# Kernel tuning notes

Measured on AMD Instinct MI355X. Metric: run time of the kernel, lower is better.

The kernel has to match this reference:

```python
import jax, jax.numpy as jnp
import numpy as np

B, T, D, H = 8, 1024, 512, 8
QD, PD, POSD, VD, K = 32, 4, 48, 64, 31
FF = 4 * D
FF1, FF2, FF3, NLA = FF * 3 // 4, FF, FF * 5 // 4, D * 3 // 4


def _swoosh_l(x):
    return jax.nn.softplus(x - 4.0) - 0.08 * x - 0.035


def _swoosh_r(x):
    return jax.nn.softplus(x - 1.0) - 0.08 * x - 0.313261687


def setup_inputs() -> dict:
    key = jax.random.key(0)
    ks = iter(jax.random.split(key, 64))

    def w(shape, fan_in):
        return jax.random.normal(next(ks), shape, jnp.float32) * (fan_in ** -0.5)

    inp = {
        'x': jax.random.normal(next(ks), (B, T, D), jnp.float32),
        'pos_emb': jax.random.normal(next(ks), (2 * T - 1, POSD), jnp.float32),
        'mask': jnp.ones((B, T), bool),
        'attw_q_w': w((D, H * QD), D), 'attw_k_w': w((D, H * QD), D),
        'attw_pq_w': w((D, H * PD), D), 'attw_pos_w': w((POSD, H * PD), POSD),
        'ff1_in_w': w((D, FF1), D), 'ff1_in_b': jnp.zeros(FF1),
        'ff1_out_w': w((FF1, D), FF1), 'ff1_out_b': jnp.zeros(D),
        'nla_w': w((D, NLA * 3), D), 'nla_b': jnp.zeros(NLA * 3),
        'nla_out_w': w((NLA, D), NLA), 'nla_out_b': jnp.zeros(D),
        'sa1_v_w': w((D, H * VD), D), 'sa1_v_b': jnp.zeros(H * VD),
        'sa1_o_w': w((H * VD, D), H * VD), 'sa1_o_b': jnp.zeros(D),
        'conv1_in_w': w((D, 2 * D), D), 'conv1_in_b': jnp.zeros(2 * D),
        'conv1_dw_w': w((D, 1, K), K), 'conv1_dw_b': jnp.zeros(D),
        'conv1_out_w': w((D, D), D), 'conv1_out_b': jnp.zeros(D),
        'ff2_in_w': w((D, FF2), D), 'ff2_in_b': jnp.zeros(FF2),
        'ff2_out_w': w((FF2, D), FF2), 'ff2_out_b': jnp.zeros(D),
        'mid_scale': jax.random.uniform(next(ks), (D,), jnp.float32),
        'sa2_v_w': w((D, H * VD), D), 'sa2_v_b': jnp.zeros(H * VD),
        'sa2_o_w': w((H * VD, D), H * VD), 'sa2_o_b': jnp.zeros(D),
        'conv2_in_w': w((D, 2 * D), D), 'conv2_in_b': jnp.zeros(2 * D),
        'conv2_dw_w': w((D, 1, K), K), 'conv2_dw_b': jnp.zeros(D),
        'conv2_out_w': w((D, D), D), 'conv2_out_b': jnp.zeros(D),
        'ff3_in_w': w((D, FF3), D), 'ff3_in_b': jnp.zeros(FF3),
        'ff3_out_w': w((FF3, D), FF3), 'ff3_out_b': jnp.zeros(D),
        'norm_bias': jnp.zeros(D), 'norm_log_scale': jnp.zeros(()),
        'out_scale': jax.random.uniform(next(ks), (D,), jnp.float32),
    }
    return inp


def _forward(x, pos_emb, attw_q_w, attw_k_w, attw_pq_w, attw_pos_w,
             ff1_in_w, ff1_in_b, ff1_out_w, ff1_out_b,
             nla_w, nla_b, nla_out_w, nla_out_b,
             sa1_v_w, sa1_v_b, sa1_o_w, sa1_o_b,
             conv1_in_w, conv1_in_b, conv1_dw_w, conv1_dw_b, conv1_out_w, conv1_out_b,
             ff2_in_w, ff2_in_b, ff2_out_w, ff2_out_b,
             mid_scale,
             sa2_v_w, sa2_v_b, sa2_o_w, sa2_o_b,
             conv2_in_w, conv2_in_b, conv2_dw_w, conv2_dw_b, conv2_out_w, conv2_out_b,
             ff3_in_w, ff3_in_b, ff3_out_w, ff3_out_b,
             norm_bias, norm_log_scale, out_scale, mask):
    res = x
    # --- relative-pos multi-head attention weights ---
    q = (x @ attw_q_w).reshape(B, T, H, QD).transpose(0, 2, 1, 3)
    k = (x @ attw_k_w).reshape(B, T, H, QD).transpose(0, 2, 1, 3)
    p = (x @ attw_pq_w).reshape(B, T, H, PD).transpose(0, 2, 1, 3)
    content = jnp.einsum('bhtd,bhsd->bhts', q, k) * (QD ** -0.5)
    rel = (pos_emb @ attw_pos_w).reshape(2 * T - 1, H, PD).transpose(1, 0, 2)
    idx = jnp.arange(T)[:, None] - jnp.arange(T)[None, :] + (T - 1)
    relg = rel[:, idx]  # [H, T, T, PD]
    scores = content + jnp.einsum('bhtd,htsd->bhts', p, relg)
    scores = jnp.where(mask[:, None, None, :], scores, -10000.0)
    attn = jax.nn.softmax(scores, axis=-1)
    attn = jnp.where(mask[:, None, :, None], attn, 0.0)

    def mk(y):
        return jnp.where(mask[..., None], y, 0.0)

    def ff(y, wi, bi, wo, bo):
        return _swoosh_l(y @ wi + bi) @ wo + bo

    def sa(y, vw, vb, ow, ob):
        v = (y @ vw + vb).reshape(B, T, H, VD).transpose(0, 2, 1, 3)
        o = jnp.einsum('bhts,bhsd->bhtd', attn, v).transpose(0, 2, 1, 3).reshape(B, T, H * VD)
        return o @ ow + ob

    def conv(y, iw, ib, dw, db, ow, ob):
        u = y @ iw + ib
        a, g = jnp.split(u, 2, axis=-1)
        a = (a * jax.nn.sigmoid(g)).transpose(0, 2, 1)  # [B, D, T]
        a = jnp.where(mask[:, None, :], a, 0.0)
        c = jax.lax.conv_general_dilated(a, dw, (1,), [(K // 2, K // 2)],
                                         dimension_numbers=('NCH', 'OIH', 'NCH'),
                                         feature_group_count=D) + db[None, :, None]
        c = _swoosh_r(c.transpose(0, 2, 1))
        return mk(c @ ow + ob)

    def bypass(r, u, s):
        s = jnp.clip(s, 0.2, 1.0)  # eval/steady regime
        return r + (u - r) * s

    x = mk(x + ff(x, ff1_in_w, ff1_in_b, ff1_out_w, ff1_out_b))
    # non-linear attention (uses head 0)
    a, b, c = jnp.split(x @ nla_w + nla_b, 3, axis=-1)
    att0 = jnp.einsum('bts,bsd->btd', attn[:, 0], jnp.tanh(b) * c)
    x = mk(x + ((a * att0) @ nla_out_w + nla_out_b))
    x = mk(x + sa(x, sa1_v_w, sa1_v_b, sa1_o_w, sa1_o_b))
    x = mk(x + conv(x, conv1_in_w, conv1_in_b, conv1_dw_w, conv1_dw_b, conv1_out_w, conv1_out_b))
    x = mk(x + ff(x, ff2_in_w, ff2_in_b, ff2_out_w, ff2_out_b))
    x = mk(bypass(res, x, mid_scale))
    x = mk(x + sa(x, sa2_v_w, sa2_v_b, sa2_o_w, sa2_o_b))
    x = mk(x + conv(x, conv2_in_w, conv2_in_b, conv2_dw_w, conv2_dw_b, conv2_out_w, conv2_out_b))
    x = mk(x + ff(x, ff3_in_w, ff3_in_b, ff3_out_w, ff3_out_b))
    # BiasNorm
    rms = jnp.sqrt(jnp.mean((x - norm_bias) ** 2, axis=-1, keepdims=True) + 1e-8)
    x = x / rms * jnp.exp(norm_log_scale)
    x = mk(bypass(res, x, out_scale))
    return x


def reference(x, pos_emb, mask, attw_q_w, attw_k_w, attw_pq_w, attw_pos_w,
              ff1_in_w, ff1_in_b, ff1_out_w, ff1_out_b,
              nla_w, nla_b, nla_out_w, nla_out_b,
              sa1_v_w, sa1_v_b, sa1_o_w, sa1_o_b,
              conv1_in_w, conv1_in_b, conv1_dw_w, conv1_dw_b, conv1_out_w, conv1_out_b,
              ff2_in_w, ff2_in_b, ff2_out_w, ff2_out_b,
              mid_scale,
              sa2_v_w, sa2_v_b, sa2_o_w, sa2_o_b,
              conv2_in_w, conv2_in_b, conv2_dw_w, conv2_dw_b, conv2_out_w, conv2_out_b,
              ff3_in_w, ff3_in_b, ff3_out_w, ff3_out_b,
              norm_bias, norm_log_scale, out_scale):
    return _forward(x, pos_emb, attw_q_w, attw_k_w, attw_pq_w, attw_pos_w,
                    ff1_in_w, ff1_in_b, ff1_out_w, ff1_out_b,
                    nla_w, nla_b, nla_out_w, nla_out_b,
                    sa1_v_w, sa1_v_b, sa1_o_w, sa1_o_b,
                    conv1_in_w, conv1_in_b, conv1_dw_w, conv1_dw_b, conv1_out_w, conv1_out_b,
                    ff2_in_w, ff2_in_b, ff2_out_w, ff2_out_b,
                    mid_scale,
                    sa2_v_w, sa2_v_b, sa2_o_w, sa2_o_b,
                    conv2_in_w, conv2_in_b, conv2_dw_w, conv2_dw_b, conv2_out_w, conv2_out_b,
                    ff3_in_w, ff3_in_b, ff3_out_w, ff3_out_b,
                    norm_bias, norm_log_scale, out_scale, mask)
```

## Files before the change

kernel.cpp:

```cpp
#include <hip/hip_runtime.h>
#include <hip/hip_bf16.h>
#include <math.h>

using bf16 = __hip_bfloat16;
using f16 = _Float16;
typedef short s16x8 __attribute__((ext_vector_type(8)));
typedef f16   f16x2 __attribute__((ext_vector_type(2)));
typedef float f32x4 __attribute__((ext_vector_type(4)));
typedef unsigned int u32;
#define DEV __device__ __forceinline__
#define AS1 __attribute__((address_space(1)))
#define AS3 __attribute__((address_space(3)))

constexpr int Bc = 8, Tc = 1024, Dc = 512, Hc = 8;
constexpr int QDc = 32, PDc = 4, POSDc = 48, VDc = 64;
constexpr int Nrow = Bc * Tc;
constexpr int KWc = 31;

DEV float frcp(float x) { return __builtin_amdgcn_rcpf(x); }
DEV float softplus_f(float y) { return fmaxf(y, 0.f) + __logf(1.f + __expf(-fabsf(y))); }
DEV float swoosh_l_f(float x) { return softplus_f(x - 4.f) - 0.08f * x - 0.035f; }
DEV float swoosh_r_f(float x) { return softplus_f(x - 1.f) - 0.08f * x - 0.313261687f; }
DEV float sigmoid_f(float x)  { return frcp(1.f + __expf(-x)); }
DEV float tanh_f(float x) {
  float e = __expf(2.f * fminf(fmaxf(x, -15.f), 15.f));
  return (e - 1.f) * frcp(e + 1.f);
}
DEV float clip_s(float s)     { return fminf(fmaxf(s, 0.2f), 1.0f); }
DEV float to_f(bf16 x)  { return __bfloat162float(x); }
DEV float b2f(short s) { union { u32 u; float f; } z; z.u = (u32)(unsigned short)s << 16; return z.f; }
DEV short f2bb(float v) { bf16 h = __float2bfloat16(v); return *(short*)&h; }
DEV unsigned short f2h(float v) { f16 h = (f16)v; union { f16 x; unsigned short s; } z; z.x = h; return z.s; }
DEV float h2f(unsigned short s) { union { unsigned short s; f16 x; } z; z.s = s; return (float)z.x; }
DEV u32 packbf(float a, float b) {
  return ((u32)(unsigned short)f2bb(b) << 16) | (u32)(unsigned short)f2bb(a);
}
DEV float dot2(u32 a, u32 b, float c) {
#if __has_builtin(__builtin_amdgcn_fdot2)
  union { u32 u; f16x2 v; } x, y; x.u = a; y.u = b;
  return __builtin_amdgcn_fdot2(x.v, y.v, c, false);
#else
  return c + h2f(a & 0xffff) * h2f(b & 0xffff) + h2f(a >> 16) * h2f(b >> 16);
#endif
}

DEV float wave_max(float v) {
#pragma unroll
  for (int o = 32; o > 0; o >>= 1) v = fmaxf(v, __shfl_xor(v, o));
  return v;
}
DEV float wave_sum(float v) {
#pragma unroll
  for (int o = 32; o > 0; o >>= 1) v += __shfl_xor(v, o);
  return v;
}

DEV void gload16(const void* g, void* l) {
  __builtin_amdgcn_global_load_lds((const AS1 u32*)g, (AS3 u32*)l, 16, 0, 0);
}

#define SWZ(a) ((a) ^ ((((a) >> 7) & 7) << 4))

template <int ACT, int WM, int WN, int FM, int FN>
__global__ __launch_bounds__(256) void gemm_mfma(
    const bf16* __restrict__ A, const bf16* __restrict__ B,
    const float* __restrict__ bias, const float* __restrict__ resid,
    float* __restrict__ Cf, bf16* __restrict__ Cb, bf16* __restrict__ Cb2,
    int M, int N, int K, int lda, int ldb, int ldc,
    long sAz, long sBo, long sBi, long sCo, long sCi, int nh) {
  constexpr int BM = WM * FM * 16, BN = WN * FN * 16;
  constexpr int NP = (ACT == 2) ? 2 : (ACT == 3) ? 3 : 1;
  constexpr int PANOFF = (ACT == 2) ? 512 : 384;
  constexpr int ASZ = BM * 128, BUF = (BM + NP * BN) * 128;
  constexpr int LPS = BM / 32 + NP * (BN / 32);

  int z = blockIdx.z;
  int zo = z / nh, zi = z - zo * nh;
  A += (long)z * sAz;
  B += (long)zo * sBo + (long)zi * sBi;
  long coff = (long)zo * sCo + (long)zi * sCi;

  __shared__ char lds[2 * BUF];

  int tid = threadIdx.x;
  int lane = tid & 63, w = tid >> 6;
  int wm = w / WN, wn = w % WN;

  int gx = gridDim.x;
  int nwg = gx * gridDim.y;
  int flat = blockIdx.y * gx + blockIdx.x;
  if ((nwg & 7) == 0) flat = (flat & 7) * (nwg >> 3) + (flat >> 3);
  int m0 = (flat / gx) * BM, n0 = (flat % gx) * BN;

  int lrow = lane >> 3, lch = lane & 7;
  const bf16* ga = A + (long)(m0 + w * (BM / 4) + lrow) * lda + ((lch ^ lrow) << 3);
  const bf16* gb = B + (long)(n0 + w * (BN / 4) + lrow) * ldb + ((lch ^ lrow) << 3);

  f32x4 acc[NP][FM][FN];
#pragma unroll
  for (int p = 0; p < NP; ++p)
#pragma unroll
    for (int i = 0; i < FM; ++i)
#pragma unroll
      for (int j = 0; j < FN; ++j) acc[p][i][j] = 0.f;

  int nt = K >> 6;
  {
    char* la = lds + w * (BM / 4) * 128;
#pragma unroll
    for (int i = 0; i < BM / 32; ++i) gload16(ga + (long)(i * 8) * lda, la + i * 1024);
#pragma unroll
    for (int p = 0; p < NP; ++p) {
      const bf16* gp = gb + (long)(p * PANOFF) * ldb;
      char* lb = lds + ASZ + p * BN * 128 + w * (BN / 4) * 128;
#pragma unroll
      for (int i = 0; i < BN / 32; ++i) gload16(gp + (long)(i * 8) * ldb, lb + i * 1024);
    }
  }

  for (int t = 0; t < nt; ++t) {
// ... 21 lines not shown
    for (int ks = 0; ks < 2; ++ks) {
      int cg = ks * 4 + (lane >> 4);
      s16x8 af[FM];
#pragma unroll
      for (int f = 0; f < FM; ++f) {
        int row = wm * FM * 16 + f * 16 + (lane & 15);
        af[f] = *(const s16x8*)(cA + row * 128 + ((cg ^ (row & 7)) << 4));
      }
#pragma unroll
      for (int p = 0; p < NP; ++p) {
        char* cB = cA + ASZ + p * BN * 128;
        s16x8 bfr[FN];
#pragma unroll
        for (int f = 0; f < FN; ++f) {
          int row = wn * FN * 16 + f * 16 + (lane & 15);
          bfr[f] = *(const s16x8*)(cB + row * 128 + ((cg ^ (row & 7)) << 4));
        }
#pragma unroll
        for (int fm = 0; fm < FM; ++fm)
#pragma unroll
          for (int fn = 0; fn < FN; ++fn)
            acc[p][fm][fn] = __builtin_amdgcn_mfma_f32_16x16x32_bf16(
                af[fm], bfr[fn], acc[p][fm][fn], 0, 0, 0);
      }
    }
    __builtin_amdgcn_sched_barrier(0);
    __builtin_amdgcn_s_barrier();
  }

  int rbase = m0 + wm * FM * 16 + (lane >> 4) * 4;
  int cbase = n0 + wn * FN * 16 + (lane & 15);
#pragma unroll
  for (int fn = 0; fn < FN; ++fn) {
    int col = cbase + fn * 16;
    if (col >= N) continue;
    float bv = bias ? bias[col] : 0.f;
#pragma unroll
    for (int fm = 0; fm < FM; ++fm) {
#pragma unroll
      for (int r = 0; r < 4; ++r) {
        int row = rbase + fm * 16 + r;
        if (row >= M) continue;
        long ci = coff + (long)row * ldc + col;
        if constexpr (ACT == 2) {
          float va = acc[0][fm][fn][r] + bv;
          float vg = acc[1][fm][fn][r] + bias[col + 512];
          Cb[ci] = __float2bfloat16(va * sigmoid_f(vg));
        } else if constexpr (ACT == 3) {
          float va = acc[0][fm][fn][r] + bv;
          float vb = acc[1][fm][fn][r] + bias[col + 384];
          float vc = acc[2][fm][fn][r] + bias[col + 768];
          Cb2[ci] = __float2bfloat16(va);
          Cb[ci] = __float2bfloat16(tanh_f(vb) * vc);
        } else {
          float v = acc[0][fm][fn][r] + bv;
          if (ACT == 1) v = swoosh_l_f(v);
          if (resid) v += resid[ci];
          if (Cf) Cf[ci] = v;
          if (Cb) Cb[ci] = __float2bfloat16(v);
        }
      }
    }
  }
}

__global__ __launch_bounds__(256) void gemm_mfma_nt(
    const bf16* __restrict__ A, const bf16* __restrict__ B,
    bf16* __restrict__ Cb, int M, int N, int K, int lda, int ldb, int ldc,
    long sAz, long sBo, long sCo) {
  int z = blockIdx.z;
  A += (long)z * sAz;
  B += (long)z * sBo;
  long coff = (long)z * sCo;

  __shared__ char lds[32768];
  char* Al = lds;
  char* Bl = lds + 16384;

  int tid = threadIdx.x;
  int lane = tid & 63, w = tid >> 6;
  int wm = w >> 1, wn = w & 1;
  int m0 = blockIdx.y * 128, n0 = blockIdx.x * 128;

  f32x4 acc[4][4];
#pragma unroll
  for (int i = 0; i < 4; ++i)
#pragma unroll
    for (int j = 0; j < 4; ++j) acc[i][j] = 0.f;

  for (int k0 = 0; k0 < K; k0 += 64) {
#pragma unroll
    for (int i = 0; i < 4; ++i) {
      int flat = tid + i * 256;
      int row = flat >> 3, ch = flat & 7;
      uint4 v = {0, 0, 0, 0};
      if (m0 + row < M)
        v = *(const uint4*)(A + (long)(m0 + row) * lda + k0 + ch * 8);
      *(uint4*)(Al + SWZ(row * 128 + ch * 16)) = v;
    }
#pragma unroll
    for (int i = 0; i < 4; ++i) {
      int flat = tid + i * 256;
      int kk = flat >> 4, nc = flat & 15;
      if (n0 + nc * 8 < N) {
        uint4 v = *(const uint4*)(B + (long)(k0 + kk) * ldb + n0 + nc * 8);
        const unsigned short* pv = (const unsigned short*)&v;
#pragma unroll
        for (int j = 0; j < 8; ++j)
          *(unsigned short*)(Bl + SWZ((nc * 8 + j) * 128 + kk * 2)) = pv[j];
      }
    }
    __syncthreads();
#pragma unroll
    for (int ks = 0; ks < 2; ++ks) {
      s16x8 af[4], bfr[4];
#pragma unroll
      for (int f = 0; f < 4; ++f)
        af[f] = *(const s16x8*)(Al + SWZ((wm * 64 + f * 16 + (lane & 15)) * 128 +
                                         ks * 64 + (lane >> 4) * 16));
#pragma unroll
      for (int f = 0; f < 4; ++f)
        bfr[f] = *(const s16x8*)(Bl + SWZ((wn * 64 + f * 16 + (lane & 15)) * 128 +
                                          ks * 64 + (lane >> 4) * 16));
#pragma unroll
      for (int fm = 0; fm < 4; ++fm)
#pragma unroll
        for (int fn = 0; fn < 4; ++fn)
          acc[fm][fn] = __builtin_amdgcn_mfma_f32_16x16x32_bf16(
              af[fm], bfr[fn], acc[fm][fn], 0, 0, 0);
    }
    __syncthreads();
  }

  int rbase = m0 + wm * 64 + (lane >> 4) * 4;
  int cbase = n0 + wn * 64 + (lane & 15);
#pragma unroll
  for (int fn = 0; fn < 4; ++fn) {
    int col = cbase + fn * 16;
    if (col >= N) continue;
#pragma unroll
    for (int fm = 0; fm < 4; ++fm) {
#pragma unroll
      for (int r = 0; r < 4; ++r) {
        int row = rbase + fm * 16 + r;
        if (row >= M) continue;
        Cb[coff + (long)row * ldc + col] = __float2bfloat16(acc[fm][fn][r]);
      }
    }
  }
}

__global__ __launch_bounds__(256) void gemm_tile_f32(
    const float* __restrict__ A, const float* __restrict__ Bm,
    float* __restrict__ Cf, f16* __restrict__ Ch,
    int M, int N, int K, int lda, int ldb, int ldc) {
  __shared__ float As[16][72];
  __shared__ float Bs[16][72];
  int tid = threadIdx.x;
  int tx = tid & 15, ty = tid >> 4;
  int m0 = blockIdx.y * 64, n0 = blockIdx.x * 64;
  int arow = tid >> 2, ak4 = (tid & 3) * 4;
  int bk = tid >> 4, bn4 = (tid & 15) * 4;
  float acc[4][4] = {};
  for (int k0 = 0; k0 < K; k0 += 16) {
    int gm = m0 + arow;
#pragma unroll
    for (int j = 0; j < 4; ++j) {
      int gk = k0 + ak4 + j;
      As[ak4 + j][arow] = (gm < M && gk < K) ? A[(long)gm * lda + gk] : 0.f;
    }
    int gk = k0 + bk;
#pragma unroll
    for (int j = 0; j < 4; ++j) {
      int gn = n0 + bn4 + j;
      Bs[bk][bn4 + j] = (gk < K && gn < N) ? Bm[(long)gk * ldb + gn] : 0.f;
    }
    __syncthreads();
#pragma unroll
    for (int kk = 0; kk < 16; ++kk) {
      float a4[4], b4[4];
#pragma unroll
      for (int i = 0; i < 4; ++i) a4[i] = As[kk][ty * 4 + i];
#pragma unroll
      for (int i = 0; i < 4; ++i) b4[i] = Bs[kk][tx * 4 + i];
#pragma unroll
      for (int i = 0; i < 4; ++i)
#pragma unroll
        for (int j = 0; j < 4; ++j) acc[i][j] += a4[i] * b4[j];
    }
    __syncthreads();
  }
#pragma unroll
  for (int i = 0; i < 4; ++i) {
    int gm = m0 + ty * 4 + i;
    if (gm >= M) continue;
#pragma unroll
    for (int j = 0; j < 4; ++j) {
      int gn = n0 + tx * 4 + j;
      if (gn < N) {
// ... 41 lines not shown
  __shared__ short t[64][72];
  int bx = blockIdx.x * 64;
  int by = blockIdx.y * 64;
  int tid = threadIdx.x;
  int r = tid >> 3, c8 = tid & 7;
#pragma unroll
  for (int p = 0; p < 2; ++p) {
    s16x8 v = *(const s16x8*)((const short*)src + (long)(bx + p * 32 + r) * C + by + c8 * 8);
#pragma unroll
    for (int j = 0; j < 8; ++j) t[p * 32 + r][c8 * 8 + j] = v[j];
  }
  __syncthreads();
  int j = tid >> 2, q = tid & 3;
  s16x8 o0, o1;
#pragma unroll
  for (int e = 0; e < 8; ++e) o0[e] = t[q * 16 + e][j];
#pragma unroll
  for (int e = 0; e < 8; ++e) o1[e] = t[q * 16 + 8 + e][j];
  short* dp = (short*)dst + (long)(by + j) * R + bx + q * 16;
  *(s16x8*)dp = o0;
  *(s16x8*)(dp + 8) = o1;
}

__global__ void dw_transpose_kernel(const float* __restrict__ dw1, float* __restrict__ o1,
                                    const float* __restrict__ dw2, float* __restrict__ o2) {
  int i = blockIdx.x * 256 + threadIdx.x;
  if (i >= 2 * 512 * KWc) return;
  const float* s = (i < 512 * KWc) ? dw1 : dw2;
  float* o = (i < 512 * KWc) ? o1 : o2;
  int j = (i < 512 * KWc) ? i : i - 512 * KWc;
  int d = j / KWc, kk = j - d * KWc;
  o[kk * 512 + d] = s[j];
}

__global__ void f2b_kernel(const float* __restrict__ in, bf16* __restrict__ out, int nOct) {
  int i = blockIdx.x * 256 + threadIdx.x;
  if (i >= nOct) return;
  float4 a = *(const float4*)(in + (long)i * 8);
  float4 b = *(const float4*)(in + (long)i * 8 + 4);
  s16x8 o;
  o[0] = f2bb(a.x); o[1] = f2bb(a.y); o[2] = f2bb(a.z); o[3] = f2bb(a.w);
  o[4] = f2bb(b.x); o[5] = f2bb(b.y); o[6] = f2bb(b.z); o[7] = f2bb(b.w);
  *(s16x8*)((short*)out + (long)i * 8) = o;
}

__global__ __launch_bounds__(256) void scores_softmax_fused(
    const bf16* __restrict__ qk, const f16* __restrict__ ph,
    const float* __restrict__ rel, bf16* __restrict__ attn) {
  int bh = blockIdx.y;
  int h = bh & (Hc - 1), b = bh >> 3;
  int t0 = blockIdx.x * 16;
  int tid = threadIdx.x, lane = tid & 63, w = tid >> 6;

  __shared__ unsigned short scS[16 * 1024];
  __shared__ u32 rel01[1040], rel23[1040];
  __shared__ u32 pS[16][2];
  __shared__ float mS[16][4];

  for (int i = tid; i < 1039; i += 256) {
    float4 rv = *(const float4*)(rel + (long)(t0 + i) * 32 + h * 4);
    rel01[i] = ((u32)f2h(rv.y) << 16) | f2h(rv.x);
    rel23[i] = ((u32)f2h(rv.w) << 16) | f2h(rv.z);
  }
  if (tid < 16) {
    const u32* pp = (const u32*)(ph + ((long)(b * Tc + t0 + tid)) * 32 + h * 4);
    pS[tid][0] = pp[0]; pS[tid][1] = pp[1];
  }
  __syncthreads();

  s16x8 af = *(const s16x8*)(qk + ((long)(b * Tc + t0 + (lane & 15))) * 512 +
                             h * QDc + (lane >> 4) * 8);
  int g = lane >> 4;
  u32 p01[4], p23[4];
#pragma unroll
  for (int r = 0; r < 4; ++r) { p01[r] = pS[g * 4 + r][0]; p23[r] = pS[g * 4 + r][1]; }
  float mx[4] = {-3e38f, -3e38f, -3e38f, -3e38f};
  f32x4 zero = {0.f, 0.f, 0.f, 0.f};
  int cols0 = w * 256;
#pragma unroll 4
  for (int tile = 0; tile < 16; ++tile) {
    int s0 = cols0 + tile * 16;
    s16x8 bfr = *(const s16x8*)(qk + ((long)(b * Tc + s0 + (lane & 15))) * 512 +
                                256 + h * QDc + (lane >> 4) * 8);
    f32x4 acc = __builtin_amdgcn_mfma_f32_16x16x32_bf16(af, bfr, zero, 0, 0, 0);
    int scol = s0 + (lane & 15);
    int idx0 = g * 4 - scol + 1023;
#pragma unroll
    for (int r = 0; r < 4; ++r) {
      int idx = idx0 + r;
      float pos = dot2(p23[r], rel23[idx], dot2(p01[r], rel01[idx], 0.f));
      float v = acc[r] + pos;
      mx[r] = fmaxf(mx[r], v);
      *(unsigned short*)((char*)scS + (g * 4 + r) * 2048 + ((scol * 2) ^ (g << 5))) = f2h(v);
    }
  }
#pragma unroll
  for (int o = 1; o < 16; o <<= 1)
#pragma unroll
    for (int r = 0; r < 4; ++r) mx[r] = fmaxf(mx[r], __shfl_xor(mx[r], o));
  if ((lane & 15) == 0) {
#pragma unroll
    for (int r = 0; r < 4; ++r) mS[g * 4 + r][w] = mx[r];
  }
  __syncthreads();

#pragma unroll
  for (int rr = 0; rr < 4; ++rr) {
    int row = w * 4 + rr;
    float mf = fmaxf(fmaxf(mS[row][0], mS[row][1]), fmaxf(mS[row][2], mS[row][3]));
    int mask = ((row >> 2) & 3) << 5;
    char* rowbase = (char*)scS + row * 2048;
    float e[16];
    float lsum = 0.f;
#pragma unroll
    for (int k = 0; k < 8; ++k) {
      u32 cw = *(u32*)(rowbase + (((lane + k * 64) * 4) ^ mask));
      float e0 = __expf(h2f(cw & 0xffff) - mf);
      float e1 = __expf(h2f(cw >> 16) - mf);
      e[k * 2] = e0; e[k * 2 + 1] = e1;
      lsum += e0 + e1;
    }
    lsum = wave_sum(lsum);
    float inv = frcp(lsum);
    u32* grow = (u32*)(attn + ((long)bh * Tc + t0 + row) * Tc);
#pragma unroll
    for (int k = 0; k < 8; ++k)
      grow[lane + k * 64] = packbf(e[k * 2] * inv, e[k * 2 + 1] * inv);
  }
}

__global__ void amul_kernel(const bf16* __restrict__ a, bf16* __restrict__ io, int nOct) {
  int i = blockIdx.x * 256 + threadIdx.x;
  if (i >= nOct) return;
  s16x8 av = *(const s16x8*)((const short*)a + (long)i * 8);
  short* p = (short*)io + (long)i * 8;
  s16x8 v = *(const s16x8*)p;
#pragma unroll
  for (int j = 0; j < 8; ++j) v[j] = f2bb(b2f(v[j]) * b2f(av[j]));
  *(s16x8*)p = v;
}

__global__ void bypass_kernel(const float* __restrict__ r, const float* __restrict__ u,
                              const float* __restrict__ s, float* __restrict__ out,
                              bf16* __restrict__ outb, int nOct) {
  int i = blockIdx.x * 256 + threadIdx.x;
  if (i >= nOct) return;
  int d0 = (i & 63) * 8;
  long base = (long)i * 8;
  float4 r0 = *(const float4*)(r + base), r1 = *(const float4*)(r + base + 4);
  float4 u0 = *(const float4*)(u + base), u1 = *(const float4*)(u + base + 4);
  float4 s0 = *(const float4*)(s + d0),  s1 = *(const float4*)(s + d0 + 4);
  float4 o0, o1;
  o0.x = r0.x + (u0.x - r0.x) * clip_s(s0.x);
  o0.y = r0.y + (u0.y - r0.y) * clip_s(s0.y);
  o0.z = r0.z + (u0.z - r0.z) * clip_s(s0.z);
  o0.w = r0.w + (u0.w - r0.w) * clip_s(s0.w);
  o1.x = r1.x + (u1.x - r1.x) * clip_s(s1.x);
  o1.y = r1.y + (u1.y - r1.y) * clip_s(s1.y);
  o1.z = r1.z + (u1.z - r1.z) * clip_s(s1.z);
  o1.w = r1.w + (u1.w - r1.w) * clip_s(s1.w);
  *(float4*)(out + base) = o0;
  *(float4*)(out + base + 4) = o1;
  s16x8 ob;
  ob[0] = f2bb(o0.x); ob[1] = f2bb(o0.y); ob[2] = f2bb(o0.z); ob[3] = f2bb(o0.w);
  ob[4] = f2bb(o1.x); ob[5] = f2bb(o1.y); ob[6] = f2bb(o1.z); ob[7] = f2bb(o1.w);
  *(s16x8*)((short*)outb + base) = ob;
}

__global__ __launch_bounds__(256) void dwconv_kernel(
    const bf16* __restrict__ a, const float* __restrict__ dwT,
    const float* __restrict__ db, bf16* __restrict__ c) {
  int i = blockIdx.x * 256 + threadIdx.x;
  int oct = i & 63, bt = i >> 6;
  int t = bt & (Tc - 1), b0 = bt - t;
  float acc0 = db[oct * 8 + 0], acc1 = db[oct * 8 + 1], acc2 = db[oct * 8 + 2],
        acc3 = db[oct * 8 + 3], acc4 = db[oct * 8 + 4], acc5 = db[oct * 8 + 5],
        acc6 = db[oct * 8 + 6], acc7 = db[oct * 8 + 7];
#pragma unroll
  for (int kk = 0; kk < KWc; ++kk) {
    int tt = t + kk - (KWc / 2);
    if ((unsigned)tt < (unsigned)Tc) {
      s16x8 av = *(const s16x8*)((const short*)a + ((long)(b0 + tt) << 9) + oct * 8);
      const float* wp = dwT + kk * 512 + oct * 8;
      float4 w0 = *(const float4*)wp, w1 = *(const float4*)(wp + 4);
      acc0 += b2f(av[0]) * w0.x; acc1 += b2f(av[1]) * w0.y;
      acc2 += b2f(av[2]) * w0.z; acc3 += b2f(av[3]) * w0.w;
      acc4 += b2f(av[4]) * w1.x; acc5 += b2f(av[5]) * w1.y;
      acc6 += b2f(av[6]) * w1.z; acc7 += b2f(av[7]) * w1.w;
    }
  }
  s16x8 o;
  o[0] = f2bb(swoosh_r_f(acc0)); o[1] = f2bb(swoosh_r_f(acc1));
  o[2] = f2bb(swoosh_r_f(acc2)); o[3] = f2bb(swoosh_r_f(acc3));
  o[4] = f2bb(swoosh_r_f(acc4)); o[5] = f2bb(swoosh_r_f(acc5));
  o[6] = f2bb(swoosh_r_f(acc6)); o[7] = f2bb(swoosh_r_f(acc7));
  *(s16x8*)((short*)c + (long)bt * 512 + oct * 8) = o;
}

__global__ __launch_bounds__(256) void rmsnorm_bypass_kernel(
    const float* __restrict__ x, const float* __restrict__ x0,
    const float* __restrict__ nb, const float* __restrict__ nls,
    const float* __restrict__ os, float* __restrict__ out) {
  int row = blockIdx.x;
  int tid = threadIdx.x;
  const float* xr = x + (long)row * 512;
  const float* rr = x0 + (long)row * 512;
  float* orow = out + (long)row * 512;
  float v0 = xr[tid], v1 = xr[tid + 256];
  float d0 = v0 - nb[tid], d1 = v1 - nb[tid + 256];
  float ss = d0 * d0 + d1 * d1;
  __shared__ float red[4];
  int lane = tid & 63, wid = tid >> 6;
  ss = wave_sum(ss);
  if (lane == 0) red[wid] = ss;
  __syncthreads();
  ss = red[0] + red[1] + red[2] + red[3];
  float rms = sqrtf(ss * (1.f / 512.f) + 1e-8f);
  float scl = expf(nls[0]) / rms;
  float r0 = rr[tid], s0 = clip_s(os[tid]);
  orow[tid] = r0 + (v0 * scl - r0) * s0;
  float r1 = rr[tid + 256], s1 = clip_s(os[tid + 256]);
  orow[tid + 256] = r1 + (v1 * scl - r1) * s1;
}

static inline int cdiv(int a, int b) { return (a + b - 1) / b; }

template <int ACT, int WM = 2, int WN = 2, int FM = 2, int FN = 2>
static void mfma_launch(hipStream_t st, const bf16* A, const bf16* B, const float* bias,
                        const float* resid, float* Cf, bf16* Cb, bf16* Cb2,
                        int M, int N, int K, int lda, int ldb, int ldc,
                        int Z = 1, int nh = 1, long sAz = 0, long sBo = 0, long sBi = 0,
                        long sCo = 0, long sCi = 0) {
  dim3 grid(cdiv(N, WN * FN * 16), cdiv(M, WM * FM * 16), Z);
  gemm_mfma<ACT, WM, WN, FM, FN><<<grid, dim3(256), 0, st>>>(
      A, B, bias, resid, Cf, Cb, Cb2, M, N, K, lda, ldb, ldc,
      sAz, sBo, sBi, sCo, sCi, nh);
}
#define MFMA_AV 4, 1, 2, 4

extern "C" void kernel_launch(void* const* d_in, const int* in_sizes, int n_in,
                              void* d_out, int out_size, void* d_ws, size_t ws_size,
                              hipStream_t stream) {
  const float* x0        = (const float*)d_in[0];
  const float* pos_emb   = (const float*)d_in[1];
  const float* Wq        = (const float*)d_in[3];
  const float* Wk        = (const float*)d_in[4];
  const float* Wpq       = (const float*)d_in[5];
  const float* Wpos      = (const float*)d_in[6];
  const float* ff1_in_w  = (const float*)d_in[7];
  const float* ff1_in_b  = (const float*)d_in[8];
  const float* ff1_out_w = (const float*)d_in[9];
  const float* ff1_out_b = (const float*)d_in[10];
  const float* nla_w     = (const float*)d_in[11];
  const float* nla_b     = (const float*)d_in[12];
  const float* nla_out_w = (const float*)d_in[13];
  const float* nla_out_b = (const float*)d_in[14];
  const float* sa1_v_w   = (const float*)d_in[15];
  const float* sa1_v_b   = (const float*)d_in[16];
  const float* sa1_o_w   = (const float*)d_in[17];
  const float* sa1_o_b   = (const float*)d_in[18];
  const float* cv1_in_w  = (const float*)d_in[19];
  const float* cv1_in_b  = (const float*)d_in[20];
  const float* cv1_dw_w  = (const float*)d_in[21];
  const float* cv1_dw_b  = (const float*)d_in[22];
  const float* cv1_out_w = (const float*)d_in[23];
  const float* cv1_out_b = (const float*)d_in[24];
  const float* ff2_in_w  = (const float*)d_in[25];
  const float* ff2_in_b  = (const float*)d_in[26];
  const float* ff2_out_w = (const float*)d_in[27];
  const float* ff2_out_b = (const float*)d_in[28];
  const float* mid_scale = (const float*)d_in[29];
  const float* sa2_v_w   = (const float*)d_in[30];
  const float* sa2_v_b   = (const float*)d_in[31];
  const float* sa2_o_w   = (const float*)d_in[32];
  const float* sa2_o_b   = (const float*)d_in[33];
  const float* cv2_in_w  = (const float*)d_in[34];
  const float* cv2_in_b  = (const float*)d_in[35];
  const float* cv2_dw_w  = (const float*)d_in[36];
  const float* cv2_dw_b  = (const float*)d_in[37];
  const float* cv2_out_w = (const float*)d_in[38];
  const float* cv2_out_b = (const float*)d_in[39];
  const float* ff3_in_w  = (const float*)d_in[40];
  const float* ff3_in_b  = (const float*)d_in[41];
  const float* ff3_out_w = (const float*)d_in[42];
  const float* ff3_out_b = (const float*)d_in[43];
  const float* norm_bias = (const float*)d_in[44];
  const float* nls       = (const float*)d_in[45];
  const float* out_scale = (const float*)d_in[46];
  float* out = (float*)d_out;

  char* wsb = (char*)d_ws;
  size_t off = 0;
  bf16* attn  = (bf16*)(wsb + off); off += (size_t)Bc * Hc * Tc * Tc * 2;
  float* xA   = (float*)(wsb + off); off += (size_t)Nrow * Dc * 4;
  float* xB   = (float*)(wsb + off); off += (size_t)Nrow * Dc * 4;
  bf16*  xb   = (bf16*)(wsb + off);  off += (size_t)Nrow * Dc * 2;
  bf16*  x0b  = (bf16*)(wsb + off);  off += (size_t)Nrow * Dc * 2;
  bf16*  big1b = (bf16*)(wsb + off); off += (size_t)Nrow * 2560 * 2;
  bf16*  big2b = (bf16*)(wsb + off); off += (size_t)Nrow * Dc * 2;
  bf16*  wT    = (bf16*)(wsb + off); off += (size_t)9961472 * 2;
  float* dwT1  = (float*)(wsb + off); off += (size_t)KWc * 512 * 4;
  float* dwT2  = (float*)(wsb + off); off += (size_t)KWc * 512 * 4;
  bf16* big3b = big1b + (size_t)Nrow * 2048;
  bf16* vT    = big2b;
  bf16* qk    = big1b;
  bf16* abuf  = big1b;
  f16*  ph    = (f16*)(big1b + (size_t)Nrow * 512);
  float* relb = (float*)(ph + (size_t)Nrow * 32);

  bf16* p_w = wT;
  auto alloc_w = [&](int n, int k) { bf16* r = p_w; p_w += (size_t)n * k; return r; };
  bf16* ff1_in_wT  = alloc_w(1536, 512);
  bf16* ff1_out_wT = alloc_w(512, 1536);
  bf16* nla_wT     = alloc_w(1152, 512);
  bf16* nla_out_wT = alloc_w(512, 384);
  bf16* sa1_v_wT   = alloc_w(512, 512);
  bf16* sa1_o_wT   = alloc_w(512, 512);
  bf16* cv1_in_wT  = alloc_w(1024, 512);
  bf16* cv1_out_wT = alloc_w(512, 512);
  bf16* ff2_in_wT  = alloc_w(2048, 512);
  bf16* ff2_out_wT = alloc_w(512, 2048);
  bf16* sa2_v_wT   = alloc_w(512, 512);
  bf16* sa2_o_wT   = alloc_w(512, 512);
  bf16* cv2_in_wT  = alloc_w(1024, 512);
  bf16* cv2_out_wT = alloc_w(512, 512);
  bf16* ff3_in_wT  = alloc_w(2560, 512);
  bf16* ff3_out_wT = alloc_w(512, 2560);
  bf16* WqkT       = alloc_w(512, 512);

  const int nOctD  = Nrow * 64;
  const int nOct384 = Nrow * 48;

  f2b_kernel<<<cdiv(nOctD, 256), 256, 0, stream>>>(x0, x0b, nOctD);
  {
    TBatch tb{};
    auto add = [&](int idx, const float* s, bf16* d, int K, int N, int& t0, float sc) {
      tb.d[idx] = {s, d, K, N, t0, cdiv(N, 32), sc};
      t0 += cdiv(N, 32) * cdiv(K, 32);
    };
    int t0 = 0;
    add(0,  ff1_in_w,  ff1_in_wT,  512, 1536, t0, 1.f);
    add(1,  ff1_out_w, ff1_out_wT, 1536, 512, t0, 1.f);
    add(2,  nla_w,     nla_wT,     512, 1152, t0, 1.f);
    add(3,  nla_out_w, nla_out_wT, 384, 512,  t0, 1.f);
    add(4,  sa1_v_w,   sa1_v_wT,   512, 512,  t0, 1.f);
    add(5,  sa1_o_w,   sa1_o_wT,   512, 512,  t0, 1.f);
    add(6,  cv1_in_w,  cv1_in_wT,  512, 1024, t0, 1.f);
    add(7,  cv1_out_w, cv1_out_wT, 512, 512,  t0, 1.f);
    add(8,  ff2_in_w,  ff2_in_wT,  512, 2048, t0, 1.f);
    add(9,  ff2_out_w, ff2_out_wT, 2048, 512, t0, 1.f);
    add(10, sa2_v_w,   sa2_v_wT,   512, 512,  t0, 1.f);
    add(11, sa2_o_w,   sa2_o_wT,   512, 512,  t0, 1.f);
    add(12, cv2_in_w,  cv2_in_wT,  512, 1024, t0, 1.f);
    add(13, cv2_out_w, cv2_out_wT, 512, 512,  t0, 1.f);
    add(14, ff3_in_w,  ff3_in_wT,  512, 2560, t0, 1.f);
    add(15, ff3_out_w, ff3_out_wT, 2560, 512, t0, 1.f);
    add(16, Wq,        WqkT,       512, 256,  t0, 0.17677669529663687f);
    add(17, Wk,        WqkT + (size_t)256 * 512, 512, 256, t0, 1.f);
    tb.n = 18;
    transpose_batch_kernel<<<t0, 256, 0, stream>>>(tb);
  }
  dw_transpose_kernel<<<cdiv(2 * 512 * KWc, 256), 256, 0, stream>>>(
      cv1_dw_w, dwT1, cv2_dw_w, dwT2);

  gemm_tile_f32<<<dim3(1, cdiv(2 * Tc - 1, 64)), 256, 0, stream>>>(
      pos_emb, Wpos, relb, nullptr, 2 * Tc - 1, 32, POSDc, POSDc, 32, 32);
  gemm_tile_f32<<<dim3(1, cdiv(Nrow, 64)), 256, 0, stream>>>(
      x0, Wpq, nullptr, ph, Nrow, 32, Dc, Dc, 32, 32);
  mfma_launch<0>(stream, x0b, WqkT, nullptr, nullptr, nullptr, qk, nullptr,
                 Nrow, 512, 512, 512, 512, 512);
  scores_softmax_fused<<<dim3(Tc / 16, 64), 256, 0, stream>>>(qk, ph, relb, attn);

  mfma_launch<1>(stream, x0b, ff1_in_wT, ff1_in_b, nullptr, nullptr, big1b, nullptr,
                 Nrow, 1536, 512, 512, 512, 1536);
  mfma_launch<0>(stream, big1b, ff1_out_wT, ff1_out_b, x0, xA, xb, nullptr,
                 Nrow, 512, 1536, 1536, 1536, 512);

  mfma_launch<3>(stream, xb, nla_wT, nla_b, nullptr, nullptr, big2b, abuf,
                 Nrow, 384, 512, 512, 512, 384);
  {
    dim3 grid(cdiv(384, 128), cdiv(Tc, 128), Bc);
    gemm_mfma_nt<<<grid, dim3(256), 0, stream>>>(
        attn, big2b, big3b, Tc, 384, Tc, Tc, 384, 384,
        (long)Hc * Tc * Tc, (long)Tc * 384, (long)Tc * 384);
  }
  amul_kernel<<<cdiv(nOct384, 256), 256, 0, stream>>>(abuf, big3b, nOct384);
  mfma_launch<0>(stream, big3b, nla_out_wT, nla_out_b, xA, xB, xb, nullptr,
                 Nrow, 512, 384, 384, 384, 512);

  mfma_launch<0>(stream, xb, sa1_v_wT, sa1_v_b, nullptr, nullptr, big3b, nullptr,
                 Nrow, 512, 512, 512, 512, 512);
  transpose_bf16_kernel<<<dim3(Nrow / 64, 8), 256, 0, stream>>>(big3b, vT, Nrow, 512);
  mfma_launch<0, MFMA_AV>(stream, attn, vT, nullptr, nullptr, nullptr, big3b, nullptr,
                          Tc, VDc, Tc, Tc, Nrow, 512,
                          Bc * Hc, Hc, (long)Tc * Tc, Tc, (long)VDc * Nrow,
                          (long)Tc * 512, VDc);
  mfma_launch<0>(stream, big3b, sa1_o_wT, sa1_o_b, xB, xA, xb, nullptr,
                 Nrow, 512, 512, 512, 512, 512);

  mfma_launch<2>(stream, xb, cv1_in_wT, cv1_in_b, nullptr, nullptr, big2b, nullptr,
                 Nrow, 512, 512, 512, 512, 512);
  dwconv_kernel<<<cdiv(nOctD, 256), 256, 0, stream>>>(big2b, dwT1, cv1_dw_b, big3b);
  mfma_launch<0>(stream, big3b, cv1_out_wT, cv1_out_b, xA, xB, xb, nullptr,
                 Nrow, 512, 512, 512, 512, 512);

  mfma_launch<1>(stream, xb, ff2_in_wT, ff2_in_b, nullptr, nullptr, big1b, nullptr,
                 Nrow, 2048, 512, 512, 512, 2048);
  mfma_launch<0>(stream, big1b, ff2_out_wT, ff2_out_b, xB, xA, nullptr, nullptr,
                 Nrow, 512, 2048, 2048, 2048, 512);

  bypass_kernel<<<cdiv(nOctD, 256), 256, 0, stream>>>(x0, xA, mid_scale, xB, xb, nOctD);

  mfma_launch<0>(stream, xb, sa2_v_wT, sa2_v_b, nullptr, nullptr, big3b, nullptr,
                 Nrow, 512, 512, 512, 512, 512);
  transpose_bf16_kernel<<<dim3(Nrow / 64, 8), 256, 0, stream>>>(big3b, vT, Nrow, 512);
  mfma_launch<0, MFMA_AV>(stream, attn, vT, nullptr, nullptr, nullptr, big3b, nullptr,
                          Tc, VDc, Tc, Tc, Nrow, 512,
                          Bc * Hc, Hc, (long)Tc * Tc, Tc, (long)VDc * Nrow,
                          (long)Tc * 512, VDc);
  mfma_launch<0>(stream, big3b, sa2_o_wT, sa2_o_b, xB, xA, xb, nullptr,
                 Nrow, 512, 512, 512, 512, 512);

  mfma_launch<2>(stream, xb, cv2_in_wT, cv2_in_b, nullptr, nullptr, big2b, nullptr,
                 Nrow, 512, 512, 512, 512, 512);
  dwconv_kernel<<<cdiv(nOctD, 256), 256, 0, stream>>>(big2b, dwT2, cv2_dw_b, big3b);
  mfma_launch<0>(stream, big3b, cv2_out_wT, cv2_out_b, xA, xB, xb, nullptr,
                 Nrow, 512, 512, 512, 512, 512);

  mfma_launch<1>(stream, xb, ff3_in_wT, ff3_in_b, nullptr, nullptr, big1b, nullptr,
                 Nrow, 2560, 512, 512, 512, 2560);
  mfma_launch<0>(stream, big1b, ff3_out_wT, ff3_out_b, xB, xA, nullptr, nullptr,
                 Nrow, 512, 2560, 2560, 2560, 512);

  rmsnorm_bypass_kernel<<<Nrow, 256, 0, stream>>>(xA, x0, norm_bias, nls, out_scale, out);
}
```

Baseline: 814.7 us.

## Fuse NLA multiply and bypass into GEMM epilogues, drop softmax max pass

The custom NT GEMM plus the separate elementwise multiply kernel for the nonlinear-attention path are replaced by a transpose followed by the standard MFMA GEMM. That GEMM gets a new epilogue (ACT 4) that multiplies by the gate buffer. The mid-block bypass kernel is folded into the ff2_out GEMM epilogue (ACT 5), which writes both fp32 and bf16 outputs in place. The score softmax now exponentiates without subtracting the row max and stores bf16 exponentials. This removes a max reduction and a reload pass, but overflows if scores grow large.

```diff
diff --git a/kernel.cpp b/kernel.cpp
--- a/kernel.cpp
+++ b/kernel.cpp
@@ -44,11 +44,6 @@
 #endif
 }
 
-DEV float wave_max(float v) {
-#pragma unroll
-  for (int o = 32; o > 0; o >>= 1) v = fmaxf(v, __shfl_xor(v, o));
-  return v;
-}
 DEV float wave_sum(float v) {
 #pragma unroll
   for (int o = 32; o > 0; o >>= 1) v += __shfl_xor(v, o);
@@ -58,14 +53,14 @@
 DEV void gload16(const void* g, void* l) {
   __builtin_amdgcn_global_load_lds((const AS1 u32*)g, (AS3 u32*)l, 16, 0, 0);
 }
-
-#define SWZ(a) ((a) ^ ((((a) >> 7) & 7) << 4))
 
 template <int ACT, int WM, int WN, int FM, int FN>
 __global__ __launch_bounds__(256) void gemm_mfma(
     const bf16* __restrict__ A, const bf16* __restrict__ B,
     const float* __restrict__ bias, const float* __restrict__ resid,
     float* __restrict__ Cf, bf16* __restrict__ Cb, bf16* __restrict__ Cb2,
+    const bf16* __restrict__ auxb, const float* __restrict__ auxf,
+    const float* __restrict__ auxf2,
     int M, int N, int K, int lda, int ldb, int ldc,
     long sAz, long sBo, long sBi, long sCo, long sCi, int nh) {
   constexpr int BM = WM * FM * 16, BN = WN * FN * 16;
@@ -193,6 +188,14 @@
           float vc = acc[2][fm][fn][r] + bias[col + 768];
           Cb2[ci] = __float2bfloat16(va);
           Cb[ci] = __float2bfloat16(tanh_f(vb) * vc);
+        } else if constexpr (ACT == 4) {
+          Cb[ci] = __float2bfloat16(acc[0][fm][fn][r] * to_f(auxb[ci]));
+        } else if constexpr (ACT == 5) {
+          float v = acc[0][fm][fn][r] + bv + resid[ci];
+          float rv = auxf[ci];
+          float o = rv + (v - rv) * clip_s(auxf2[col]);
+          Cf[ci] = o;
+          Cb[ci] = __float2bfloat16(o);
         } else {
           float v = acc[0][fm][fn][r] + bv;
           if (ACT == 1) v = swoosh_l_f(v);
@@ -200,92 +203,6 @@
           if (Cf) Cf[ci] = v;
           if (Cb) Cb[ci] = __float2bfloat16(v);
         }
-      }
-    }
-  }
-}
-
-__global__ __launch_bounds__(256) void gemm_mfma_nt(
-    const bf16* __restrict__ A, const bf16* __restrict__ B,
-    bf16* __restrict__ Cb, int M, int N, int K, int lda, int ldb, int ldc,
-    long sAz, long sBo, long sCo) {
-  int z = blockIdx.z;
-  A += (long)z * sAz;
-  B += (long)z * sBo;
-  long coff = (long)z * sCo;
-
-  __shared__ char lds[32768];
-  char* Al = lds;
-  char* Bl = lds + 16384;
-
-  int tid = threadIdx.x;
-  int lane = tid & 63, w = tid >> 6;
-  int wm = w >> 1, wn = w & 1;
-  int m0 = blockIdx.y * 128, n0 = blockIdx.x * 128;
-
-  f32x4 acc[4][4];
-#pragma unroll
-  for (int i = 0; i < 4; ++i)
-#pragma unroll
-    for (int j = 0; j < 4; ++j) acc[i][j] = 0.f;
-
-  for (int k0 = 0; k0 < K; k0 += 64) {
-#pragma unroll
-    for (int i = 0; i < 4; ++i) {
-      int flat = tid + i * 256;
-      int row = flat >> 3, ch = flat & 7;
-      uint4 v = {0, 0, 0, 0};
-      if (m0 + row < M)
-        v = *(const uint4*)(A + (long)(m0 + row) * lda + k0 + ch * 8);
-      *(uint4*)(Al + SWZ(row * 128 + ch * 16)) = v;
-    }
-#pragma unroll
-    for (int i = 0; i < 4; ++i) {
-      int flat = tid + i * 256;
-      int kk = flat >> 4, nc = flat & 15;
-      if (n0 + nc * 8 < N) {
-        uint4 v = *(const uint4*)(B + (long)(k0 + kk) * ldb + n0 + nc * 8);
-        const unsigned short* pv = (const unsigned short*)&v;
-#pragma unroll
-        for (int j = 0; j < 8; ++j)
-          *(unsigned short*)(Bl + SWZ((nc * 8 + j) * 128 + kk * 2)) = pv[j];
-      }
-    }
-    __syncthreads();
-#pragma unroll
-    for (int ks = 0; ks < 2; ++ks) {
-      s16x8 af[4], bfr[4];
-#pragma unroll
-      for (int f = 0; f < 4; ++f)
-        af[f] = *(const s16x8*)(Al + SWZ((wm * 64 + f * 16 + (lane & 15)) * 128 +
-                                         ks * 64 + (lane >> 4) * 16));
-#pragma unroll
-      for (int f = 0; f < 4; ++f)
-        bfr[f] = *(const s16x8*)(Bl + SWZ((wn * 64 + f * 16 + (lane & 15)) * 128 +
-                                          ks * 64 + (lane >> 4) * 16));
-#pragma unroll
-      for (int fm = 0; fm < 4; ++fm)
-#pragma unroll
-        for (int fn = 0; fn < 4; ++fn)
-          acc[fm][fn] = __builtin_amdgcn_mfma_f32_16x16x32_bf16(
-              af[fm], bfr[fn], acc[fm][fn], 0, 0, 0);
-    }
-    __syncthreads();
-  }
-
-  int rbase = m0 + wm * 64 + (lane >> 4) * 4;
-  int cbase = n0 + wn * 64 + (lane & 15);
-#pragma unroll
-  for (int fn = 0; fn < 4; ++fn) {
-    int col = cbase + fn * 16;
-    if (col >= N) continue;
-#pragma unroll
-    for (int fm = 0; fm < 4; ++fm) {
-#pragma unroll
-      for (int r = 0; r < 4; ++r) {
-        int row = rbase + fm * 16 + r;
-        if (row >= M) continue;
-        Cb[coff + (long)row * ldc + col] = __float2bfloat16(acc[fm][fn][r]);
       }
     }
   }
@@ -433,10 +350,10 @@
   int t0 = blockIdx.x * 16;
   int tid = threadIdx.x, lane = tid & 63, w = tid >> 6;
 
-  __shared__ unsigned short scS[16 * 1024];
+  __shared__ unsigned short eS[16 * 1024];
   __shared__ u32 rel01[1040], rel23[1040];
   __shared__ u32 pS[16][2];
-  __shared__ float mS[16][4];
+  __shared__ float lS[16][4];
 
   for (int i = tid; i < 1039; i += 256) {
     float4 rv = *(const float4*)(rel + (long)(t0 + i) * 32 + h * 4);
@@ -455,7 +372,7 @@
   u32 p01[4], p23[4];
 #pragma unroll
   for (int r = 0; r < 4; ++r) { p01[r] = pS[g * 4 + r][0]; p23[r] = pS[g * 4 + r][1]; }
-  float mx[4] = {-3e38f, -3e38f, -3e38f, -3e38f};
+  float sum[4] = {0.f, 0.f, 0.f, 0.f};
   f32x4 zero = {0.f, 0.f, 0.f, 0.f};
   int cols0 = w * 256;
 #pragma unroll 4
@@ -470,82 +387,36 @@
     for (int r = 0; r < 4; ++r) {
       int idx = idx0 + r;
       float pos = dot2(p23[r], rel23[idx], dot2(p01[r], rel01[idx], 0.f));
-      float v = acc[r] + pos;
-      mx[r] = fmaxf(mx[r], v);
-      *(unsigned short*)((char*)scS + (g * 4 + r) * 2048 + ((scol * 2) ^ (g << 5))) = f2h(v);
+      float e = __expf(acc[r] + pos);
+      sum[r] += e;
+      *(unsigned short*)((char*)eS + (g * 4 + r) * 2048 + ((scol * 2) ^ (g << 5))) =
+          (unsigned short)f2bb(e);
     }
   }
 #pragma unroll
   for (int o = 1; o < 16; o <<= 1)
 #pragma unroll
-    for (int r = 0; r < 4; ++r) mx[r] = fmaxf(mx[r], __shfl_xor(mx[r], o));
+    for (int r = 0; r < 4; ++r) sum[r] += __shfl_xor(sum[r], o);
   if ((lane & 15) == 0) {
 #pragma unroll
-    for (int r = 0; r < 4; ++r) mS[g * 4 + r][w] = mx[r];
+    for (int r = 0; r < 4; ++r) lS[g * 4 + r][w] = sum[r];
   }
   __syncthreads();
 
 #pragma unroll
   for (int rr = 0; rr < 4; ++rr) {
     int row = w * 4 + rr;
-    float mf = fmaxf(fmaxf(mS[row][0], mS[row][1]), fmaxf(mS[row][2], mS[row][3]));
+    float inv = frcp(lS[row][0] + lS[row][1] + lS[row][2] + lS[row][3]);
     int mask = ((row >> 2) & 3) << 5;
-    char* rowbase = (char*)scS + row * 2048;
-    float e[16];
-    float lsum = 0.f;
+    char* rowbase = (char*)eS + row * 2048;
+    u32* grow = (u32*)(attn + ((long)bh * Tc + t0 + row) * Tc);
 #pragma unroll
     for (int k = 0; k < 8; ++k) {
-      u32 cw = *(u32*)(rowbase + (((lane + k * 64) * 4) ^ mask));
-      float e0 = __expf(h2f(cw & 0xffff) - mf);
-      float e1 = __expf(h2f(cw >> 16) - mf);
-      e[k * 2] = e0; e[k * 2 + 1] = e1;
-      lsum += e0 + e1;
-    }
-    lsum = wave_sum(lsum);
-    float inv = frcp(lsum);
-    u32* grow = (u32*)(attn + ((long)bh * Tc + t0 + row) * Tc);
-#pragma unroll
-    for (int k = 0; k < 8; ++k)
-      grow[lane + k * 64] = packbf(e[k * 2] * inv, e[k * 2 + 1] * inv);
-  }
-}
-
-__global__ void amul_kernel(const bf16* __restrict__ a, bf16* __restrict__ io, int nOct) {
-  int i = blockIdx.x * 256 + threadIdx.x;
-  if (i >= nOct) return;
-  s16x8 av = *(const s16x8*)((const short*)a + (long)i * 8);
-  short* p = (short*)io + (long)i * 8;
-  s16x8 v = *(const s16x8*)p;
-#pragma unroll
-  for (int j = 0; j < 8; ++j) v[j] = f2bb(b2f(v[j]) * b2f(av[j]));
-  *(s16x8*)p = v;
-}
-
-__global__ void bypass_kernel(const float* __restrict__ r, const float* __restrict__ u,
-                              const float* __restrict__ s, float* __restrict__ out,
-                              bf16* __restrict__ outb, int nOct) {
-  int i = blockIdx.x * 256 + threadIdx.x;
-  if (i >= nOct) return;
-  int d0 = (i & 63) * 8;
-  long base = (long)i * 8;
-  float4 r0 = *(const float4*)(r + base), r1 = *(const float4*)(r + base + 4);
-  float4 u0 = *(const float4*)(u + base), u1 = *(const float4*)(u + base + 4);
-  float4 s0 = *(const float4*)(s + d0),  s1 = *(const float4*)(s + d0 + 4);
-  float4 o0, o1;
-  o0.x = r0.x + (u0.x - r0.x) * clip_s(s0.x);
-  o0.y = r0.y + (u0.y - r0.y) * clip_s(s0.y);
-  o0.z = r0.z + (u0.z - r0.z) * clip_s(s0.z);
-  o0.w = r0.w + (u0.w - r0.w) * clip_s(s0.w);
-  o1.x = r1.x + (u1.x - r1.x) * clip_s(s1.x);
-  o1.y = r1.y + (u1.y - r1.y) * clip_s(s1.y);
-  o1.z = r1.z + (u1.z - r1.z) * clip_s(s1.z);
-  o1.w = r1.w + (u1.w - r1.w) * clip_s(s1.w);
-  *(float4*)(out + base) = o0;
-  *(float4*)(out + base + 4) = o1;
-  s16x8 ob;
-  ob[0] = f2bb(o0.x); ob[1] = f2bb(o0.y); ob[2] = f2bb(o0.z); ob[3] = f2bb(o0.w);
-  ob[4] = f2bb(o1.x); ob[5] = f2bb(o1.y); ob[6] = f2bb(o1.z); ob[7] = f2bb(o1.w);
-  *(s16x8*)((short*)outb + base) = ob;
+      u32 ew = *(u32*)(rowbase + (((lane + k * 64) * 4) ^ mask));
+      grow[lane + k * 64] = packbf(b2f((short)(ew & 0xffff)) * inv,
+                                   b2f((short)(ew >> 16)) * inv);
+    }
+  }
 }
 
 __global__ __launch_bounds__(256) void dwconv_kernel(
@@ -609,12 +480,13 @@
 template <int ACT, int WM = 2, int WN = 2, int FM = 2, int FN = 2>
 static void mfma_launch(hipStream_t st, const bf16* A, const bf16* B, const float* bias,
                         const float* resid, float* Cf, bf16* Cb, bf16* Cb2,
+                        const bf16* auxb, const float* auxf, const float* auxf2,
                         int M, int N, int K, int lda, int ldb, int ldc,
                         int Z = 1, int nh = 1, long sAz = 0, long sBo = 0, long sBi = 0,
                         long sCo = 0, long sCi = 0) {
   dim3 grid(cdiv(N, WN * FN * 16), cdiv(M, WM * FM * 16), Z);
   gemm_mfma<ACT, WM, WN, FM, FN><<<grid, dim3(256), 0, st>>>(
-      A, B, bias, resid, Cf, Cb, Cb2, M, N, K, lda, ldb, ldc,
+      A, B, bias, resid, Cf, Cb, Cb2, auxb, auxf, auxf2, M, N, K, lda, ldb, ldc,
       sAz, sBo, sBi, sCo, sCi, nh);
 }
 #define MFMA_AV 4, 1, 2, 4
@@ -682,6 +554,7 @@
   bf16*  wT    = (bf16*)(wsb + off); off += (size_t)9961472 * 2;
   float* dwT1  = (float*)(wsb + off); off += (size_t)KWc * 512 * 4;
   float* dwT2  = (float*)(wsb + off); off += (size_t)KWc * 512 * 4;
+  bf16*  tbcT  = (bf16*)(wsb + off); off += (size_t)384 * Nrow * 2;
   bf16* big3b = big1b + (size_t)Nrow * 2048;
   bf16* vT    = big2b;
   bf16* qk    = big1b;
@@ -709,8 +582,7 @@
   bf16* ff3_out_wT = alloc_w(512, 2560);
   bf16* WqkT       = alloc_w(512, 512);
 
-  const int nOctD  = Nrow * 64;
-  const int nOct384 = Nrow * 48;
+  const int nOctD = Nrow * 64;
 
   f2b_kernel<<<cdiv(nOctD, 256), 256, 0, stream>>>(x0, x0b, nOctD);
   {
@@ -749,69 +621,65 @@
   gemm_tile_f32<<<dim3(1, cdiv(Nrow, 64)), 256, 0, stream>>>(
       x0, Wpq, nullptr, ph, Nrow, 32, Dc, Dc, 32, 32);
   mfma_launch<0>(stream, x0b, WqkT, nullptr, nullptr, nullptr, qk, nullptr,
-                 Nrow, 512, 512, 512, 512, 512);
+                 nullptr, nullptr, nullptr, Nrow, 512, 512, 512, 512, 512);
   scores_softmax_fused<<<dim3(Tc / 16, 64), 256, 0, stream>>>(qk, ph, relb, attn);
 
   mfma_launch<1>(stream, x0b, ff1_in_wT, ff1_in_b, nullptr, nullptr, big1b, nullptr,
-                 Nrow, 1536, 512, 512, 512, 1536);
+                 nullptr, nullptr, nullptr, Nrow, 1536, 512, 512, 512, 1536);
   mfma_launch<0>(stream, big1b, ff1_out_wT, ff1_out_b, x0, xA, xb, nullptr,
-                 Nrow, 512, 1536, 1536, 1536, 512);
+                 nullptr, nullptr, nullptr, Nrow, 512, 1536, 1536, 1536, 512);
 
   mfma_launch<3>(stream, xb, nla_wT, nla_b, nullptr, nullptr, big2b, abuf,
-                 Nrow, 384, 512, 512, 512, 384);
-  {
-    dim3 grid(cdiv(384, 128), cdiv(Tc, 128), Bc);
-    gemm_mfma_nt<<<grid, dim3(256), 0, stream>>>(
-        attn, big2b, big3b, Tc, 384, Tc, Tc, 384, 384,
-        (long)Hc * Tc * Tc, (long)Tc * 384, (long)Tc * 384);
-  }
-  amul_kernel<<<cdiv(nOct384, 256), 256, 0, stream>>>(abuf, big3b, nOct384);
+                 nullptr, nullptr, nullptr, Nrow, 384, 512, 512, 512, 384);
+  transpose_bf16_kernel<<<dim3(Nrow / 64, 384 / 64), 256, 0, stream>>>(
+      big2b, tbcT, Nrow, 384);
+  mfma_launch<4>(stream, attn, tbcT, nullptr, nullptr, nullptr, big3b, nullptr,
+                 abuf, nullptr, nullptr, Tc, 384, Tc, Tc, Nrow, 384,
+                 Bc, 1, (long)Hc * Tc * Tc, 1024, 0, (long)Tc * 384, 0);
   mfma_launch<0>(stream, big3b, nla_out_wT, nla_out_b, xA, xB, xb, nullptr,
-                 Nrow, 512, 384, 384, 384, 512);
+                 nullptr, nullptr, nullptr, Nrow, 512, 384, 384, 384, 512);
 
   mfma_launch<0>(stream, xb, sa1_v_wT, sa1_v_b, nullptr, nullptr, big3b, nullptr,
-                 Nrow, 512, 512, 512, 512, 512);
+                 nullptr, nullptr, nullptr, Nrow, 512, 512, 512, 512, 512);
   transpose_bf16_kernel<<<dim3(Nrow / 64, 8), 256, 0, stream>>>(big3b, vT, Nrow, 512);
   mfma_launch<0, MFMA_AV>(stream, attn, vT, nullptr, nullptr, nullptr, big3b, nullptr,
-                          Tc, VDc, Tc, Tc, Nrow, 512,
+                          nullptr, nullptr, nullptr, Tc, VDc, Tc, Tc, Nrow, 512,
                           Bc * Hc, Hc, (long)Tc * Tc, Tc, (long)VDc * Nrow,
                           (long)Tc * 512, VDc);
   mfma_launch<0>(stream, big3b, sa1_o_wT, sa1_o_b, xB, xA, xb, nullptr,
-                 Nrow, 512, 512, 512, 512, 512);
+                 nullptr, nullptr, nullptr, Nrow, 512, 512, 512, 512, 512);
 
   mfma_launch<2>(stream, xb, cv1_in_wT, cv1_in_b, nullptr, nullptr, big2b, nullptr,
-                 Nrow, 512, 512, 512, 512, 512);
+                 nullptr, nullptr, nullptr, Nrow, 512, 512, 512, 512, 512);
   dwconv_kernel<<<cdiv(nOctD, 256), 256, 0, stream>>>(big2b, dwT1, cv1_dw_b, big3b);
   mfma_launch<0>(stream, big3b, cv1_out_wT, cv1_out_b, xA, xB, xb, nullptr,
-                 Nrow, 512, 512, 512, 512, 512);
+                 nullptr, nullptr, nullptr, Nrow, 512, 512, 512, 512, 512);
 
   mfma_launch<1>(stream, xb, ff2_in_wT, ff2_in_b, nullptr, nullptr, big1b, nullptr,
-                 Nrow, 2048, 512, 512, 512, 2048);
-  mfma_launch<0>(stream, big1b, ff2_out_wT, ff2_out_b, xB, xA, nullptr, nullptr,
-                 Nrow, 512, 2048, 2048, 2048, 512);
-
-  bypass_kernel<<<cdiv(nOctD, 256), 256, 0, stream>>>(x0, xA, mid_scale, xB, xb, nOctD);
+                 nullptr, nullptr, nullptr, Nrow, 2048, 512, 512, 512, 2048);
+  mfma_launch<5>(stream, big1b, ff2_out_wT, ff2_out_b, xB, xB, xb, nullptr,
+                 nullptr, x0, mid_scale, Nrow, 512, 2048, 2048, 2048, 512);
 
   mfma_launch<0>(stream, xb, sa2_v_wT, sa2_v_b, nullptr, nullptr, big3b, nullptr,
-                 Nrow, 512, 512, 512, 512, 512);
+                 nullptr, nullptr, nullptr, Nrow, 512, 512, 512, 512, 512);
   transpose_bf16_kernel<<<dim3(Nrow / 64, 8), 256, 0, stream>>>(big3b, vT, Nrow, 512);
   mfma_launch<0, MFMA_AV>(stream, attn, vT, nullptr, nullptr, nullptr, big3b, nullptr,
-                          Tc, VDc, Tc, Tc, Nrow, 512,
+                          nullptr, nullptr, nullptr, Tc, VDc, Tc, Tc, Nrow, 512,
                           Bc * Hc, Hc, (long)Tc * Tc, Tc, (long)VDc * Nrow,
                           (long)Tc * 512, VDc);
   mfma_launch<0>(stream, big3b, sa2_o_wT, sa2_o_b, xB, xA, xb, nullptr,
-                 Nrow, 512, 512, 512, 512, 512);
+                 nullptr, nullptr, nullptr, Nrow, 512, 512, 512, 512, 512);
 
   mfma_launch<2>(stream, xb, cv2_in_wT, cv2_in_b, nullptr, nullptr, big2b, nullptr,
-                 Nrow, 512, 512, 512, 512, 512);
+                 nullptr, nullptr, nullptr, Nrow, 512, 512, 512, 512, 512);
   dwconv_kernel<<<cdiv(nOctD, 256), 256, 0, stream>>>(big2b, dwT2, cv2_dw_b, big3b);
   mfma_launch<0>(stream, big3b, cv2_out_wT, cv2_out_b, xA, xB, xb, nullptr,
-                 Nrow, 512, 512, 512, 512, 512);
+                 nullptr, nullptr, nullptr, Nrow, 512, 512, 512, 512, 512);
 
   mfma_launch<1>(stream, xb, ff3_in_wT, ff3_in_b, nullptr, nullptr, big1b, nullptr,
-                 Nrow, 2560, 512, 512, 512, 2560);
+                 nullptr, nullptr, nullptr, Nrow, 2560, 512, 512, 512, 2560);
   mfma_launch<0>(stream, big1b, ff3_out_wT, ff3_out_b, xB, xA, nullptr, nullptr,
-                 Nrow, 512, 2560, 2560, 2560, 512);
+                 nullptr, nullptr, nullptr, Nrow, 512, 2560, 2560, 2560, 512);
 
   rmsnorm_bypass_kernel<<<Nrow, 256, 0, stream>>>(xA, x0, norm_bias, nls, out_scale, out);
 }
```

Result: faster. 767.6 us (-5.8%).
